# Optimization experiments

Measured on AMD Instinct MI355X. Metric: run time of the kernel, lower is better.

The kernel has to match this reference:

```python
import jax, jax.numpy as jnp
import numpy as np

N = 8192
D_IN = 128
D_HID = 256  # hard-coded nn.Linear(input_dim, 256) in the module
D_OUT = 64
BN_EPS = 1e-5
LEAKY_SLOPE = 0.01


def setup_inputs() -> dict:
    key = jax.random.key(0)
    k_h, k_a, k_wt, k_wo = jax.random.split(key, 4)
    H = jax.random.normal(k_h, (N, D_IN), dtype=jnp.float32)
    # Fixed adjacency passed to __init__; values in [0,1) so mask=ceil(A*1e-5) is {0,1}
    A = jax.random.uniform(k_a, (N, N), dtype=jnp.float32)
    bn_weight = jnp.ones((D_IN,), jnp.float32)
    bn_bias = jnp.zeros((D_IN,), jnp.float32)
    W_theta = jax.random.normal(k_wt, (D_IN, D_HID), jnp.float32) * np.float32(1.0 / np.sqrt(D_IN))
    b_theta = jnp.zeros((D_HID,), jnp.float32)
    W_out = jax.random.normal(k_wo, (D_IN, D_OUT), jnp.float32) * np.float32(1.0 / np.sqrt(D_IN))
    b_out = jnp.zeros((D_OUT,), jnp.float32)
    return {"H": H, "A": A, "bn_weight": bn_weight, "bn_bias": bn_bias,
            "W_theta": W_theta, "b_theta": b_theta, "W_out": W_out, "b_out": b_out}


def reference(H, A, bn_weight, bn_bias, W_theta, b_theta, W_out, b_out):
    # BatchNorm1d in training mode: biased batch statistics over the node dim
    mean = jnp.mean(H, axis=0)
    var = jnp.mean(jnp.square(H - mean), axis=0)
    Hn = (H - mean) * jax.lax.rsqrt(var + BN_EPS) * bn_weight + bn_bias  # [N, D_IN]

    Hx = Hn @ W_theta + b_theta  # [N, 256]
    mask = jnp.ceil(A * 1e-5)    # constant {0,1} mask from fixed adjacency

    # Dynamic adjacency: clamp(sigmoid(Hx Hx^T), min=0.1) * mask + I
    S = jnp.clip(jax.nn.sigmoid(Hx @ Hx.T), 0.1, None)  # [N, N]
    Ad = S * mask + jnp.eye(N, dtype=H.dtype)

    # D^{-1/2} A D^{-1/2} via broadcast scaling (same math as diag matmuls)
    d = jax.lax.rsqrt(jnp.sum(Ad, axis=1))  # D^{-0.5}, [N]
    A_hat = Ad * d[:, None] * d[None, :]

    out = A_hat @ (Hn @ W_out + b_out)       # [N, D_OUT]
    out = jnp.where(out >= 0, out, LEAKY_SLOPE * out)  # LeakyReLU(0.01)
    return out, A_hat
```

## Files before the change

### kernel.cpp

```cpp
#include <hip/hip_runtime.h>
#include <hip/hip_bf16.h>

#define N 8192
#define DIN 128
#define DHID 256
#define DOUT 64
#define VP 136

typedef __attribute__((ext_vector_type(8))) short short8;
typedef __attribute__((ext_vector_type(8))) unsigned short u16x8;
typedef __attribute__((ext_vector_type(4))) float f32x4;
typedef __attribute__((ext_vector_type(2))) unsigned long long u64x2;

typedef __attribute__((address_space(1))) const unsigned int GlbU32;
typedef __attribute__((address_space(3))) unsigned int LdsU32;

__device__ inline void gload16(const void* g, void* l) {
  __builtin_amdgcn_global_load_lds((GlbU32*)g, (LdsU32*)l, 16, 0, 0);
}

#define LGKM_BAR()                                            \
  do {                                                        \
    asm volatile("s_waitcnt lgkmcnt(0)" ::: "memory");        \
    __builtin_amdgcn_sched_barrier(0);                        \
    __builtin_amdgcn_s_barrier();                             \
    __builtin_amdgcn_sched_barrier(0);                        \
  } while (0)

__device__ inline unsigned short f2bf(float x) {
  unsigned u = __float_as_uint(x);
  u += 0x7FFF + ((u >> 16) & 1);
  return (unsigned short)(u >> 16);
}
__device__ inline float sig_clip(float x) {
  float s = 1.0f / (1.0f + __expf(-x));
  return fmaxf(s, 0.1f);
}

__global__ __launch_bounds__(256) void maskpack(const float* __restrict__ A,
                                                unsigned long long* __restrict__ Mb) {
  size_t i = (size_t)blockIdx.x * 256 + threadIdx.x;
  size_t step = (size_t)gridDim.x * 256;
  int l = threadIdx.x & 63;
  for (; i < (size_t)N * N / 4; i += step) {
    f32x4 a = *(const f32x4*)&A[i * 4];
    unsigned long long b0 = __ballot(a[0] > 0.f);
    unsigned long long b1 = __ballot(a[1] > 0.f);
    unsigned long long b2 = __ballot(a[2] > 0.f);
    unsigned long long b3 = __ballot(a[3] > 0.f);
    size_t g = (i - l) >> 6;
    if (l < 4) {
      unsigned long long bb = (l == 0) ? b0 : (l == 1) ? b1 : (l == 2) ? b2 : b3;
      Mb[g * 4 + l] = bb;
    }
  }
}

__global__ void bn_stats(const float* __restrict__ H, const float* __restrict__ bnw,
                         const float* __restrict__ bnb, float* __restrict__ scale,
                         float* __restrict__ shift) {
  int f = blockIdx.x;
  int t = threadIdx.x;
  float s = 0.f, sq = 0.f;
  for (int r = t; r < N; r += 256) {
    float v = H[(size_t)r * DIN + f];
    s += v; sq += v * v;
  }
  __shared__ float ss[256], s2[256];
  ss[t] = s; s2[t] = sq;
  __syncthreads();
  for (int o = 128; o > 0; o >>= 1) {
    if (t < o) { ss[t] += ss[t + o]; s2[t] += s2[t + o]; }
    __syncthreads();
  }
  if (t == 0) {
    float mean = ss[0] * (1.0f / N);
    float var = s2[0] * (1.0f / N) - mean * mean;
    float sc = rsqrtf(var + 1e-5f) * bnw[f];
    scale[f] = sc;
    shift[f] = bnb[f] - mean * sc;
  }
}

__global__ __launch_bounds__(256) void proj(const float* __restrict__ H,
                     const float* __restrict__ scale, const float* __restrict__ shift,
                     const float* __restrict__ Wt, const float* __restrict__ bt,
                     const float* __restrict__ Wo, const float* __restrict__ bo,
                     unsigned short* __restrict__ Hx, unsigned short* __restrict__ M2T) {
  __shared__ float hn[8][DIN];
  int i0 = blockIdx.x * 8;
  int t = threadIdx.x;
  #pragma unroll
  for (int rep = 0; rep < 4; ++rep) {
    int idx = rep * 256 + t;
    int r = idx >> 7, c = idx & 127;
    float h = H[(size_t)(i0 + r) * DIN + c];
    hn[r][c] = fmaf(h, scale[c], shift[c]);
  }
  __syncthreads();
  {
    int c = t;
    float acc[8];
    float b = bt[c];
    #pragma unroll
    for (int r = 0; r < 8; ++r) acc[r] = b;
    for (int k = 0; k < DIN; ++k) {
      float w = Wt[k * DHID + c];
      #pragma unroll
      for (int r = 0; r < 8; ++r) acc[r] = fmaf(hn[r][k], w, acc[r]);
    }
    #pragma unroll
    for (int r = 0; r < 8; ++r) Hx[(size_t)(i0 + r) * DHID + c] = f2bf(acc[r]);
  }
  if (t < DOUT) {
    int c = t;
    float acc[8];
    float b = bo[c];
    #pragma unroll
    for (int r = 0; r < 8; ++r) acc[r] = b;
    for (int k = 0; k < DIN; ++k) {
      float w = Wo[k * DOUT + c];
      #pragma unroll
      for (int r = 0; r < 8; ++r) acc[r] = fmaf(hn[r][k], w, acc[r]);
    }
    u16x8 v;
    #pragma unroll
    for (int r = 0; r < 8; ++r) v[r] = f2bf(acc[r]);
    *(u16x8*)&M2T[(size_t)c * N + i0] = v;
  }
}

__global__ __launch_bounds__(256) void rsum(const unsigned short* __restrict__ Hx,
                     const unsigned long long* __restrict__ Mb,
                     float* __restrict__ rowsum) {
  int jt = blockIdx.x, it = blockIdx.y;
  if (jt < it) return;
  __shared__ unsigned short lsh[16384];
  __shared__ unsigned mbt32[128][4];
  __shared__ unsigned mbtT[128][4];
  __shared__ float scs[4][128];
  unsigned short* la = lsh;
  unsigned short* lb = lsh + 8192;
  int i0 = it * 128, j0 = jt * 128;
  int t = threadIdx.x;
  int w = t >> 6, l = t & 63;
  int lr = l & 15, lg = l >> 4;
  const bool offdiag = (it != jt);

  if (t < 128) {
    const unsigned long long* src = &Mb[(size_t)(i0 + t) * (N / 64) + (j0 >> 8) * 4];
    int sh = (j0 & 128) ? 32 : 0;
    #pragma unroll
    for (int e = 0; e < 4; ++e)
      mbt32[t][e] = (unsigned)(src[e] >> sh);
  }
  if (offdiag && t < 128) {
    const unsigned long long* srcT = &Mb[(size_t)(j0 + t) * (N / 64) + (i0 >> 8) * 4];
    int shT = (i0 & 128) ? 32 : 0;
    #pragma unroll
    for (int e = 0; e < 4; ++e)
      mbtT[t][e] = (unsigned)(srcT[e] >> shT);
  }

  f32x4 acc[2][8];
  f32x4 zero = {0.f, 0.f, 0.f, 0.f};
  #pragma unroll
  for (int m = 0; m < 2; ++m)
    #pragma unroll
    for (int n = 0; n < 8; ++n) acc[m][n] = zero;

  const int srow = l >> 3;
  const int scol = ((l & 7) ^ srow) * 8;
  const int fswz = (lr & 7) * 8;

  for (int c4 = 0; c4 < 4; ++c4) {
    int k0 = c4 * 64;
    __syncthreads();
    #pragma unroll
    for (int rp = 0; rp < 4; ++rp) {
      int chunk = rp * 4 + w;
      int row = chunk * 8 + srow;
      gload16(&Hx[(size_t)(i0 + row) * DHID + k0 + scol], &la[chunk * 512]);
      gload16(&Hx[(size_t)(j0 + row) * DHID + k0 + scol], &lb[chunk * 512]);
    }
    __syncthreads();
    #pragma unroll
    for (int kk = 0; kk < 2; ++kk) {
      int c = (kk * 32 + lg * 8) ^ fswz;
      short8 af[2], bf[8];
      #pragma unroll
      for (int m = 0; m < 2; ++m)
        af[m] = *(const short8*)&la[(w * 32 + m * 16 + lr) * 64 + c];
      #pragma unroll
      for (int n = 0; n < 8; ++n)
        bf[n] = *(const short8*)&lb[(n * 16 + lr) * 64 + c];
      #pragma unroll
      for (int m = 0; m < 2; ++m)
        #pragma unroll
        for (int n = 0; n < 8; ++n)
          acc[m][n] = __builtin_amdgcn_mfma_f32_16x16x32_bf16(af[m], bf[n], acc[m][n], 0, 0, 0);
    }
  }

  #pragma unroll
  for (int m = 0; m < 2; ++m) {
    #pragma unroll
    for (int r = 0; r < 4; ++r) {
      int rl = w * 32 + m * 16 + lg * 4 + r;
      int gi = i0 + rl;
      unsigned mw = mbt32[rl][lr & 3];
      float part = 0.f;
      #pragma unroll
      for (int n = 0; n < 8; ++n) {
        int gj = j0 + n * 16 + lr;
        float ms = ((mw >> (n * 4 + (lr >> 2))) & 1u) ? 1.f : 0.f;
        part += sig_clip(acc[m][n][r]) * ms + (gi == gj ? 1.f : 0.f);
      }
      part += __shfl_xor(part, 1);
      part += __shfl_xor(part, 2);
      part += __shfl_xor(part, 4);
      part += __shfl_xor(part, 8);
      if (lr == 0) atomicAdd(&rowsum[gi], part);
    }
  }

  if (offdiag) {
    float p[8];
    #pragma unroll
    for (int n = 0; n < 8; ++n) p[n] = 0.f;
    #pragma unroll
    for (int m = 0; m < 2; ++m) {
      #pragma unroll
      for (int r = 0; r < 4; ++r) {
        int bitp = w * 8 + m * 4 + lg;
        #pragma unroll
        for (int n = 0; n < 8; ++n) {
          int c = n * 16 + lr;
          float ms = ((mbtT[c][r] >> bitp) & 1u) ? 1.f : 0.f;
          p[n] += sig_clip(acc[m][n][r]) * ms;
        }
      }
    }
    #pragma unroll
    for (int n = 0; n < 8; ++n) {
      p[n] += __shfl_xor(p[n], 16);
      p[n] += __shfl_xor(p[n], 32);
    }
    if (lg == 0) {
      #pragma unroll
      for (int n = 0; n < 8; ++n) scs[w][n * 16 + lr] = p[n];
    }
    __syncthreads();
    if (t < 128) {
      float cs = scs[0][t] + scs[1][t] + scs[2][t] + scs[3][t];
      atomicAdd(&rowsum[j0 + t], cs);
    }
  }
}

__global__ void dfin(float* rs) {
  int i = blockIdx.x * 256 + threadIdx.x;
  if (i < N) rs[i] = rsqrtf(rs[i]);
}

__global__ __launch_bounds__(256) void finmm(const unsigned short* __restrict__ Hx,
                     const unsigned long long* __restrict__ Mb,
                     const float* __restrict__ dd,
                     const unsigned short* __restrict__ M2T,
                     float* __restrict__ Ahat, float* __restrict__ out) {
  __shared__ unsigned short lsh[25600];
  __shared__ unsigned mbt32[128][4];
  unsigned short* lb = lsh;
  unsigned short* lVb = lsh + 8192;
  const int blk = blockIdx.x;
  const int jq = blk & 7;
  const int it = blk >> 3;
  const int i0 = it * 128;
  const int t = threadIdx.x;
  const int w = t >> 6, l = t & 63;
  const int lr = l & 15, lg = l >> 4;
  const int srow = l >> 3;
  const int scol = ((l & 7) ^ srow) * 8;
  const int fswz = (lr & 7) * 8;

  short8 af[2][8];
  #pragma unroll
  for (int h = 0; h < 2; ++h) {
    __syncthreads();
    #pragma unroll
    for (int itr = 0; itr < 8; ++itr) {
      int idx = itr * 4 + w;
      int c4 = idx >> 3, rg = idx & 7;
      int row = h * 64 + rg * 8 + srow;
      gload16(&Hx[(size_t)(i0 + row) * DHID + c4 * 64 + scol], &lsh[idx * 512]);
    }
    __syncthreads();
    if ((w >> 1) == h) {
      #pragma unroll
      for (int c4 = 0; c4 < 4; ++c4)
        #pragma unroll
        for (int kk = 0; kk < 2; ++kk)
          #pragma unroll
          for (int m = 0; m < 2; ++m)
            af[m][c4 * 2 + kk] = *(const short8*)&lsh[c4 * 4096 +
                ((w & 1) * 32 + m * 16 + lr) * 64 + ((kk * 32 + lg * 8) ^ fswz)];
    }
  }
  __syncthreads();

  float di[2][4];
  #pragma unroll
  for (int m = 0; m < 2; ++m)
    #pragma unroll
    for (int r = 0; r < 4; ++r)
      di[m][r] = dd[i0 + w * 32 + m * 16 + lg * 4 + r];

  {
    int j0 = jq * 8 * 128;
    int mrow = t >> 1, ep = (t & 1) * 2;
    u64x2 mv = *(const u64x2*)&Mb[(size_t)(i0 + mrow) * (N / 64) + (j0 >> 8) * 4 + ep];
    int sh = (j0 & 128) ? 32 : 0;
    mbt32[mrow][ep] = (unsigned)(mv[0] >> sh);
    mbt32[mrow][ep + 1] = (unsigned)(mv[1] >> sh);
  }

  f32x4 acc2[2][4];
  f32x4 zero = {0.f, 0.f, 0.f, 0.f};
  #pragma unroll
  for (int m = 0; m < 2; ++m)
    #pragma unroll
    for (int n = 0; n < 4; ++n) acc2[m][n] = zero;

  for (int jtl = 0; jtl < 8; ++jtl) {
    const int j0 = (jq * 8 + jtl) * 128;
    f32x4 acc[2][8];
    #pragma unroll
    for (int m = 0; m < 2; ++m)
      #pragma unroll
      for (int n = 0; n < 8; ++n) acc[m][n] = zero;

    #pragma unroll
    for (int c4 = 0; c4 < 4; ++c4) {
      __syncthreads();
      #pragma unroll
      for (int itr = 0; itr < 4; ++itr) {
        int rg = itr * 4 + w;
        int row = rg * 8 + srow;
        gload16(&Hx[(size_t)(j0 + row) * DHID + c4 * 64 + scol], &lb[rg * 512]);
      }
      __syncthreads();
      #pragma unroll
      for (int kk = 0; kk < 2; ++kk) {
        int c = (kk * 32 + lg * 8) ^ fswz;
        short8 bf[8];
        #pragma unroll
        for (int n = 0; n < 8; ++n)
          bf[n] = *(const short8*)&lb[(n * 16 + lr) * 64 + c];
        #pragma unroll
        for (int m = 0; m < 2; ++m)
          #pragma unroll
          for (int n = 0; n < 8; ++n)
            acc[m][n] = __builtin_amdgcn_mfma_f32_16x16x32_bf16(af[m][c4 * 2 + kk], bf[n], acc[m][n], 0, 0, 0);
      }
    }

    float dj[8];
    #pragma unroll
    for (int n = 0; n < 8; ++n) dj[n] = dd[j0 + n * 16 + lr];
    #pragma unroll
    for (int m = 0; m < 2; ++m) {
      #pragma unroll
      for (int r = 0; r < 4; ++r) {
        int rl = w * 32 + m * 16 + lg * 4 + r;
        int gi = i0 + rl;
        unsigned mw = mbt32[rl][lr & 3];
        #pragma unroll
        for (int n = 0; n < 8; ++n) {
          int gj = j0 + n * 16 + lr;
          float ms = ((mw >> (n * 4 + (lr >> 2))) & 1u) ? 1.f : 0.f;
          float v = sig_clip(acc[m][n][r]) * ms + (gi == gj ? 1.f : 0.f);
          float a = v * di[m][r] * dj[n];
          Ahat[(size_t)gi * N + gj] = a;
          lVb[rl * VP + n * 16 + lr] = f2bf(a);
        }
      }
    }
    LGKM_BAR();

    #pragma unroll
    for (int kk2 = 0; kk2 < 4; ++kk2) {
      short8 af2[2], bfr[4];
      #pragma unroll
      for (int m = 0; m < 2; ++m)
        af2[m] = *(const short8*)&lVb[(w * 32 + m * 16 + lr) * VP + kk2 * 32 + lg * 8];
      #pragma unroll
      for (int n = 0; n < 4; ++n)
        bfr[n] = *(const short8*)&M2T[(size_t)(n * 16 + lr) * N + j0 + kk2 * 32 + lg * 8];
      #pragma unroll
      for (int m = 0; m < 2; ++m)
        #pragma unroll
        for (int n = 0; n < 4; ++n)
          acc2[m][n] = __builtin_amdgcn_mfma_f32_16x16x32_bf16(af2[m], bfr[n], acc2[m][n], 0, 0, 0);
    }

    if (jtl < 7) {
      int nj0 = (jq * 8 + jtl + 1) * 128;
      int mrow = t >> 1, ep = (t & 1) * 2;
      u64x2 mv = *(const u64x2*)&Mb[(size_t)(i0 + mrow) * (N / 64) + (nj0 >> 8) * 4 + ep];
      int sh = (nj0 & 128) ? 32 : 0;
      mbt32[mrow][ep] = (unsigned)(mv[0] >> sh);
      mbt32[mrow][ep + 1] = (unsigned)(mv[1] >> sh);
    }
  }

  #pragma unroll
  for (int m = 0; m < 2; ++m)
    #pragma unroll
    for (int n = 0; n < 4; ++n)
      #pragma unroll
      for (int r = 0; r < 4; ++r) {
        int gi = i0 + w * 32 + m * 16 + lg * 4 + r;
        int gc = n * 16 + lr;
        atomicAdd(&out[(size_t)gi * DOUT + gc], acc2[m][n][r]);
      }
}

__global__ void leaky(float* out) {
  int i = blockIdx.x * 256 + threadIdx.x;
  if (i < N * DOUT) {
    float x = out[i];
    out[i] = x >= 0.f ? x : 0.01f * x;
  }
}

extern "C" void kernel_launch(void* const* d_in, const int* in_sizes, int n_in,
                              void* d_out, int out_size, void* d_ws, size_t ws_size,
                              hipStream_t stream) {
  const float* H   = (const float*)d_in[0];
  const float* A   = (const float*)d_in[1];
  const float* bnw = (const float*)d_in[2];
  const float* bnb = (const float*)d_in[3];
  const float* Wt  = (const float*)d_in[4];
  const float* bt  = (const float*)d_in[5];
  const float* Wo  = (const float*)d_in[6];
  const float* bo  = (const float*)d_in[7];
  float* out = (float*)d_out;
  float* Ahat = out + (size_t)N * DOUT;

  char* ws = (char*)d_ws;
  float* scale  = (float*)(ws + 0);
  float* shift  = (float*)(ws + 512);
  float* rowsum = (float*)(ws + 4096);
  unsigned short* M2T = (unsigned short*)(ws + 65536);
  unsigned short* Hx  = (unsigned short*)(ws + 2097152);
  unsigned long long* Mb = (unsigned long long*)(ws + (size_t)(6u << 20));

  hipMemsetAsync(rowsum, 0, N * sizeof(float), stream);
  hipMemsetAsync(out, 0, (size_t)N * DOUT * sizeof(float), stream);

  maskpack<<<4096, 256, 0, stream>>>(A, Mb);
  bn_stats<<<DIN, 256, 0, stream>>>(H, bnw, bnb, scale, shift);
  proj<<<N / 8, 256, 0, stream>>>(H, scale, shift, Wt, bt, Wo, bo, Hx, M2T);
  rsum<<<dim3(64, 64), 256, 0, stream>>>(Hx, Mb, rowsum);
  dfin<<<N / 256, 256, 0, stream>>>(rowsum);
  finmm<<<512, 256, 0, stream>>>(Hx, Mb, rowsum, M2T, Ahat, out);
  leaky<<<(N * DOUT + 255) / 256, 256, 0, stream>>>(out);
}
```

Baseline: 373.4 us.

## Stage A_hat tiles in LDS for vector stores and restructure rowsum kernel

The finmm kernel no longer writes A_hat with scattered scalar stores from MFMA fragments. It reads back the bf16 tile it already builds in LDS and writes each row as contiguous 128-bit float stores. The rowsum kernel now uses finmm's row-block layout: A-side fragments are kept in registers, each block loops over 8 column tiles, and row partials are accumulated before a single atomic per row. This drops the symmetric upper-triangle trick and its column-sum atomics, so that kernel does twice the MFMA work. finmm's grid grows to 1024 blocks of 4 column tiles each. A_hat is now written from bf16-rounded values, which lowers output precision.

```diff
diff --git a/kernel.cpp b/kernel.cpp
--- a/kernel.cpp
+++ b/kernel.cpp
@@ -31,6 +31,9 @@
   unsigned u = __float_as_uint(x);
   u += 0x7FFF + ((u >> 16) & 1);
   return (unsigned short)(u >> 16);
+}
+__device__ inline float bf2f(unsigned short u) {
+  return __uint_as_float(((unsigned)u) << 16);
 }
 __device__ inline float sig_clip(float x) {
   float s = 1.0f / (1.0f + __expf(-x));
@@ -133,145 +136,9 @@
 __global__ __launch_bounds__(256) void rsum(const unsigned short* __restrict__ Hx,
                      const unsigned long long* __restrict__ Mb,
                      float* __restrict__ rowsum) {
-  int jt = blockIdx.x, it = blockIdx.y;
-  if (jt < it) return;
   __shared__ unsigned short lsh[16384];
   __shared__ unsigned mbt32[128][4];
-  __shared__ unsigned mbtT[128][4];
-  __shared__ float scs[4][128];
-  unsigned short* la = lsh;
-  unsigned short* lb = lsh + 8192;
-  int i0 = it * 128, j0 = jt * 128;
-  int t = threadIdx.x;
-  int w = t >> 6, l = t & 63;
-  int lr = l & 15, lg = l >> 4;
-  const bool offdiag = (it != jt);
-
-  if (t < 128) {
-    const unsigned long long* src = &Mb[(size_t)(i0 + t) * (N / 64) + (j0 >> 8) * 4];
-    int sh = (j0 & 128) ? 32 : 0;
-    #pragma unroll
-    for (int e = 0; e < 4; ++e)
-      mbt32[t][e] = (unsigned)(src[e] >> sh);
-  }
-  if (offdiag && t < 128) {
-    const unsigned long long* srcT = &Mb[(size_t)(j0 + t) * (N / 64) + (i0 >> 8) * 4];
-    int shT = (i0 & 128) ? 32 : 0;
-    #pragma unroll
-    for (int e = 0; e < 4; ++e)
-      mbtT[t][e] = (unsigned)(srcT[e] >> shT);
-  }
-
-  f32x4 acc[2][8];
-  f32x4 zero = {0.f, 0.f, 0.f, 0.f};
-  #pragma unroll
-  for (int m = 0; m < 2; ++m)
-    #pragma unroll
-    for (int n = 0; n < 8; ++n) acc[m][n] = zero;
-
-  const int srow = l >> 3;
-  const int scol = ((l & 7) ^ srow) * 8;
-  const int fswz = (lr & 7) * 8;
-
-  for (int c4 = 0; c4 < 4; ++c4) {
-    int k0 = c4 * 64;
-    __syncthreads();
-    #pragma unroll
-    for (int rp = 0; rp < 4; ++rp) {
-      int chunk = rp * 4 + w;
-      int row = chunk * 8 + srow;
-      gload16(&Hx[(size_t)(i0 + row) * DHID + k0 + scol], &la[chunk * 512]);
-      gload16(&Hx[(size_t)(j0 + row) * DHID + k0 + scol], &lb[chunk * 512]);
-    }
-    __syncthreads();
-    #pragma unroll
-    for (int kk = 0; kk < 2; ++kk) {
-      int c = (kk * 32 + lg * 8) ^ fswz;
-      short8 af[2], bf[8];
-      #pragma unroll
-      for (int m = 0; m < 2; ++m)
-        af[m] = *(const short8*)&la[(w * 32 + m * 16 + lr) * 64 + c];
-      #pragma unroll
-      for (int n = 0; n < 8; ++n)
-        bf[n] = *(const short8*)&lb[(n * 16 + lr) * 64 + c];
-      #pragma unroll
-      for (int m = 0; m < 2; ++m)
-        #pragma unroll
-        for (int n = 0; n < 8; ++n)
-          acc[m][n] = __builtin_amdgcn_mfma_f32_16x16x32_bf16(af[m], bf[n], acc[m][n], 0, 0, 0);
-    }
-  }
-
-  #pragma unroll
-  for (int m = 0; m < 2; ++m) {
-    #pragma unroll
-    for (int r = 0; r < 4; ++r) {
-      int rl = w * 32 + m * 16 + lg * 4 + r;
-      int gi = i0 + rl;
-      unsigned mw = mbt32[rl][lr & 3];
-      float part = 0.f;
-      #pragma unroll
-      for (int n = 0; n < 8; ++n) {
-        int gj = j0 + n * 16 + lr;
-        float ms = ((mw >> (n * 4 + (lr >> 2))) & 1u) ? 1.f : 0.f;
-        part += sig_clip(acc[m][n][r]) * ms + (gi == gj ? 1.f : 0.f);
-      }
-      part += __shfl_xor(part, 1);
-      part += __shfl_xor(part, 2);
-      part += __shfl_xor(part, 4);
-      part += __shfl_xor(part, 8);
-      if (lr == 0) atomicAdd(&rowsum[gi], part);
-    }
-  }
-
-  if (offdiag) {
-    float p[8];
-    #pragma unroll
-    for (int n = 0; n < 8; ++n) p[n] = 0.f;
-    #pragma unroll
-    for (int m = 0; m < 2; ++m) {
-      #pragma unroll
-      for (int r = 0; r < 4; ++r) {
-        int bitp = w * 8 + m * 4 + lg;
-        #pragma unroll
-        for (int n = 0; n < 8; ++n) {
-          int c = n * 16 + lr;
-          float ms = ((mbtT[c][r] >> bitp) & 1u) ? 1.f : 0.f;
-          p[n] += sig_clip(acc[m][n][r]) * ms;
-        }
-      }
-    }
-    #pragma unroll
-    for (int n = 0; n < 8; ++n) {
-      p[n] += __shfl_xor(p[n], 16);
-      p[n] += __shfl_xor(p[n], 32);
-    }
-    if (lg == 0) {
-      #pragma unroll
-      for (int n = 0; n < 8; ++n) scs[w][n * 16 + lr] = p[n];
-    }
-    __syncthreads();
-    if (t < 128) {
-      float cs = scs[0][t] + scs[1][t] + scs[2][t] + scs[3][t];
-      atomicAdd(&rowsum[j0 + t], cs);
-    }
-  }
-}
-
-__global__ void dfin(float* rs) {
-  int i = blockIdx.x * 256 + threadIdx.x;
-  if (i < N) rs[i] = rsqrtf(rs[i]);
-}
-
-__global__ __launch_bounds__(256) void finmm(const unsigned short* __restrict__ Hx,
-                     const unsigned long long* __restrict__ Mb,
-                     const float* __restrict__ dd,
-                     const unsigned short* __restrict__ M2T,
-                     float* __restrict__ Ahat, float* __restrict__ out) {
-  __shared__ unsigned short lsh[25600];
-  __shared__ unsigned mbt32[128][4];
   unsigned short* lb = lsh;
-  unsigned short* lVb = lsh + 8192;
   const int blk = blockIdx.x;
   const int jq = blk & 7;
   const int it = blk >> 3;
@@ -308,13 +175,6 @@
   }
   __syncthreads();
 
-  float di[2][4];
-  #pragma unroll
-  for (int m = 0; m < 2; ++m)
-    #pragma unroll
-    for (int r = 0; r < 4; ++r)
-      di[m][r] = dd[i0 + w * 32 + m * 16 + lg * 4 + r];
-
   {
     int j0 = jq * 8 * 128;
     int mrow = t >> 1, ep = (t & 1) * 2;
@@ -324,6 +184,149 @@
     mbt32[mrow][ep + 1] = (unsigned)(mv[1] >> sh);
   }
 
+  float rs[2][4] = {{0.f, 0.f, 0.f, 0.f}, {0.f, 0.f, 0.f, 0.f}};
+  f32x4 zero = {0.f, 0.f, 0.f, 0.f};
+
+  for (int jtl = 0; jtl < 8; ++jtl) {
+    const int j0 = (jq * 8 + jtl) * 128;
+    f32x4 acc[2][8];
+    #pragma unroll
+    for (int m = 0; m < 2; ++m)
+      #pragma unroll
+      for (int n = 0; n < 8; ++n) acc[m][n] = zero;
+
+    #pragma unroll
+    for (int c4 = 0; c4 < 4; ++c4) {
+      __syncthreads();
+      #pragma unroll
+      for (int itr = 0; itr < 4; ++itr) {
+        int rg = itr * 4 + w;
+        int row = rg * 8 + srow;
+        gload16(&Hx[(size_t)(j0 + row) * DHID + c4 * 64 + scol], &lb[rg * 512]);
+      }
+      __syncthreads();
+      #pragma unroll
+      for (int kk = 0; kk < 2; ++kk) {
+        int c = (kk * 32 + lg * 8) ^ fswz;
+        short8 bf[8];
+        #pragma unroll
+        for (int n = 0; n < 8; ++n)
+          bf[n] = *(const short8*)&lb[(n * 16 + lr) * 64 + c];
+        #pragma unroll
+        for (int m = 0; m < 2; ++m)
+          #pragma unroll
+          for (int n = 0; n < 8; ++n)
+            acc[m][n] = __builtin_amdgcn_mfma_f32_16x16x32_bf16(af[m][c4 * 2 + kk], bf[n], acc[m][n], 0, 0, 0);
+      }
+    }
+
+    #pragma unroll
+    for (int m = 0; m < 2; ++m) {
+      #pragma unroll
+      for (int r = 0; r < 4; ++r) {
+        int rl = w * 32 + m * 16 + lg * 4 + r;
+        int gi = i0 + rl;
+        unsigned mw = mbt32[rl][lr & 3];
+        float part = 0.f;
+        #pragma unroll
+        for (int n = 0; n < 8; ++n) {
+          int gj = j0 + n * 16 + lr;
+          float ms = ((mw >> (n * 4 + (lr >> 2))) & 1u) ? 1.f : 0.f;
+          part += sig_clip(acc[m][n][r]) * ms + (gi == gj ? 1.f : 0.f);
+        }
+        rs[m][r] += part;
+      }
+    }
+    __syncthreads();
+    if (jtl < 7) {
+      int nj0 = (jq * 8 + jtl + 1) * 128;
+      int mrow = t >> 1, ep = (t & 1) * 2;
+      u64x2 mv = *(const u64x2*)&Mb[(size_t)(i0 + mrow) * (N / 64) + (nj0 >> 8) * 4 + ep];
+      int sh = (nj0 & 128) ? 32 : 0;
+      mbt32[mrow][ep] = (unsigned)(mv[0] >> sh);
+      mbt32[mrow][ep + 1] = (unsigned)(mv[1] >> sh);
+    }
+  }
+
+  #pragma unroll
+  for (int m = 0; m < 2; ++m)
+    #pragma unroll
+    for (int r = 0; r < 4; ++r) {
+      float p = rs[m][r];
+      p += __shfl_xor(p, 1);
+      p += __shfl_xor(p, 2);
+      p += __shfl_xor(p, 4);
+      p += __shfl_xor(p, 8);
+      if (lr == 0) atomicAdd(&rowsum[i0 + w * 32 + m * 16 + lg * 4 + r], p);
+    }
+}
+
+__global__ void dfin(float* rs) {
+  int i = blockIdx.x * 256 + threadIdx.x;
+  if (i < N) rs[i] = rsqrtf(rs[i]);
+}
+
+__global__ __launch_bounds__(256) void finmm(const unsigned short* __restrict__ Hx,
+                     const unsigned long long* __restrict__ Mb,
+                     const float* __restrict__ dd,
+                     const unsigned short* __restrict__ M2T,
+                     float* __restrict__ Ahat, float* __restrict__ out) {
+  __shared__ unsigned short lsh[21504];
+  __shared__ unsigned mbt32[128][4];
+  unsigned short* lb = lsh;
+  unsigned short* lVb = lsh + 4096;
+  const int blk = blockIdx.x;
+  const int jq = blk & 15;
+  const int it = blk >> 4;
+  const int i0 = it * 128;
+  const int t = threadIdx.x;
+  const int w = t >> 6, l = t & 63;
+  const int lr = l & 15, lg = l >> 4;
+  const int srow = l >> 3;
+  const int scol = ((l & 7) ^ srow) * 8;
+  const int fswz = (lr & 7) * 8;
+
+  short8 af[2][8];
+  #pragma unroll
+  for (int h = 0; h < 2; ++h) {
+    __syncthreads();
+    #pragma unroll
+    for (int itr = 0; itr < 8; ++itr) {
+      int idx = itr * 4 + w;
+      int c4 = idx >> 3, rg = idx & 7;
+      int row = h * 64 + rg * 8 + srow;
+      gload16(&Hx[(size_t)(i0 + row) * DHID + c4 * 64 + scol], &lsh[idx * 512]);
+    }
+    __syncthreads();
+    if ((w >> 1) == h) {
+      #pragma unroll
+      for (int c4 = 0; c4 < 4; ++c4)
+        #pragma unroll
+        for (int kk = 0; kk < 2; ++kk)
+          #pragma unroll
+          for (int m = 0; m < 2; ++m)
+            af[m][c4 * 2 + kk] = *(const short8*)&lsh[c4 * 4096 +
+                ((w & 1) * 32 + m * 16 + lr) * 64 + ((kk * 32 + lg * 8) ^ fswz)];
+    }
+  }
+  __syncthreads();
+
+  float di[2][4];
+  #pragma unroll
+  for (int m = 0; m < 2; ++m)
+    #pragma unroll
+    for (int r = 0; r < 4; ++r)
+      di[m][r] = dd[i0 + w * 32 + m * 16 + lg * 4 + r];
+
+  {
+    int j0 = jq * 4 * 128;
+    int mrow = t >> 1, ep = (t & 1) * 2;
+    u64x2 mv = *(const u64x2*)&Mb[(size_t)(i0 + mrow) * (N / 64) + (j0 >> 8) * 4 + ep];
+    int sh = (j0 & 128) ? 32 : 0;
+    mbt32[mrow][ep] = (unsigned)(mv[0] >> sh);
+    mbt32[mrow][ep + 1] = (unsigned)(mv[1] >> sh);
+  }
+
   f32x4 acc2[2][4];
   f32x4 zero = {0.f, 0.f, 0.f, 0.f};
   #pragma unroll
@@ -331,8 +334,8 @@
     #pragma unroll
     for (int n = 0; n < 4; ++n) acc2[m][n] = zero;
 
-  for (int jtl = 0; jtl < 8; ++jtl) {
-    const int j0 = (jq * 8 + jtl) * 128;
+  for (int jtl = 0; jtl < 4; ++jtl) {
+    const int j0 = (jq * 4 + jtl) * 128;
     f32x4 acc[2][8];
     #pragma unroll
     for (int m = 0; m < 2; ++m)
@@ -380,7 +383,6 @@
           float ms = ((mw >> (n * 4 + (lr >> 2))) & 1u) ? 1.f : 0.f;
           float v = sig_clip(acc[m][n][r]) * ms + (gi == gj ? 1.f : 0.f);
           float a = v * di[m][r] * dj[n];
-          Ahat[(size_t)gi * N + gj] = a;
           lVb[rl * VP + n * 16 + lr] = f2bf(a);
         }
       }
@@ -388,6 +390,19 @@
     LGKM_BAR();
 
     #pragma unroll
+    for (int pass = 0; pass < 8; ++pass) {
+      int row = pass * 16 + (t >> 4);
+      int cc = (t & 15) * 8;
+      u16x8 vv = *(const u16x8*)&lVb[row * VP + cc];
+      f32x4 o0, o1;
+      o0[0] = bf2f(vv[0]); o0[1] = bf2f(vv[1]); o0[2] = bf2f(vv[2]); o0[3] = bf2f(vv[3]);
+      o1[0] = bf2f(vv[4]); o1[1] = bf2f(vv[5]); o1[2] = bf2f(vv[6]); o1[3] = bf2f(vv[7]);
+      size_t idx = (size_t)(i0 + row) * N + j0 + cc;
+      *(f32x4*)&Ahat[idx] = o0;
+      *(f32x4*)&Ahat[idx + 4] = o1;
+    }
+
+    #pragma unroll
     for (int kk2 = 0; kk2 < 4; ++kk2) {
       short8 af2[2], bfr[4];
       #pragma unroll
@@ -403,8 +418,8 @@
           acc2[m][n] = __builtin_amdgcn_mfma_f32_16x16x32_bf16(af2[m], bfr[n], acc2[m][n], 0, 0, 0);
     }
 
-    if (jtl < 7) {
-      int nj0 = (jq * 8 + jtl + 1) * 128;
+    if (jtl < 3) {
+      int nj0 = (jq * 4 + jtl + 1) * 128;
       int mrow = t >> 1, ep = (t & 1) * 2;
       u64x2 mv = *(const u64x2*)&Mb[(size_t)(i0 + mrow) * (N / 64) + (nj0 >> 8) * 4 + ep];
       int sh = (nj0 & 128) ? 32 : 0;
@@ -461,8 +476,8 @@
   maskpack<<<4096, 256, 0, stream>>>(A, Mb);
   bn_stats<<<DIN, 256, 0, stream>>>(H, bnw, bnb, scale, shift);
   proj<<<N / 8, 256, 0, stream>>>(H, scale, shift, Wt, bt, Wo, bo, Hx, M2T);
-  rsum<<<dim3(64, 64), 256, 0, stream>>>(Hx, Mb, rowsum);
+  rsum<<<512, 256, 0, stream>>>(Hx, Mb, rowsum);
   dfin<<<N / 256, 256, 0, stream>>>(rowsum);
-  finmm<<<512, 256, 0, stream>>>(Hx, Mb, rowsum, M2T, Ahat, out);
+  finmm<<<1024, 256, 0, stream>>>(Hx, Mb, rowsum, M2T, Ahat, out);
   leaky<<<(N * DOUT + 255) / 256, 256, 0, stream>>>(out);
 }
```

New measurement: 420.4 us. 1.13x slower.
